# Performance work log

Hardware: AMD Instinct MI355X
Metric: run time of the kernel (lower is better)

The kernel has to match this reference:

```python
import jax, jax.numpy as jnp
import numpy as np

B, T, C, HS = 4, 2048, 2048, 64
H = C // HS
LW, LA, LV, LG = 64, 64, 32, 128
EPS_GN = 0.00064


def setup_inputs() -> dict:
    key = jax.random.key(0)
    ks = jax.random.split(key, 32)
    rn = lambda k, shape, s=1.0: jax.random.normal(k, shape, dtype=jnp.float32) * s
    return {
        "x": rn(ks[0], (B, T, C)),
        "v_first": rn(ks[1], (B, T, C)),
        "x_prev": rn(ks[2], (B, C)),
        "wkv_state": rn(ks[3], (B, H, HS, HS), 0.1),
        "x_r": rn(ks[4], (C,), 0.1),
        "x_w": rn(ks[5], (C,), 0.1),
        "x_k": rn(ks[6], (C,), 0.1),
        "x_v": rn(ks[7], (C,), 0.1),
        "x_a": rn(ks[8], (C,), 0.1),
        "x_g": rn(ks[9], (C,), 0.1),
        "w0": rn(ks[10], (C,), 0.1),
        "w1": rn(ks[11], (C, LW), 0.02),
        "w2": rn(ks[12], (LW, C), 0.02),
        "a0": rn(ks[13], (C,), 0.1),
        "a1": rn(ks[14], (C, LA), 0.02),
        "a2": rn(ks[15], (LA, C), 0.02),
        "v0": rn(ks[16], (C,), 0.1),
        "v1": rn(ks[17], (C, LV), 0.02),
        "v2": rn(ks[18], (LV, C), 0.02),
        "g1": rn(ks[19], (C, LG), 0.02),
        "g2": rn(ks[20], (LG, C), 0.02),
        "k_k": rn(ks[21], (C,), 0.1),
        "k_a": rn(ks[22], (C,), 0.1),
        "r_k": rn(ks[23], (H, HS), 0.1),
        "Wr": rn(ks[24], (C, C), 0.02),
        "Wk": rn(ks[25], (C, C), 0.02),
        "Wv": rn(ks[26], (C, C), 0.02),
        "Wo": rn(ks[27], (C, C), 0.02),
        "ln_w": jnp.ones((C,), dtype=jnp.float32),
        "ln_b": jnp.zeros((C,), dtype=jnp.float32),
    }


def _fwd(x, v_first, x_prev, wkv_state, x_r, x_w, x_k, x_v, x_a, x_g,
         w0, w1, w2, a0, a1, a2, v0, v1, v2, g1, g2, k_k, k_a, r_k,
         Wr, Wk, Wv, Wo, ln_w, ln_b):
    Bb, Tt, Cc = x.shape
    # token shift
    xx = jnp.concatenate([x_prev[:, None, :], x[:, :-1, :]], axis=1) - x
    xr = x + xx * x_r; xw = x + xx * x_w; xk = x + xx * x_k
    xv = x + xx * x_v; xa = x + xx * x_a; xg = x + xx * x_g
    r = xr @ Wr
    k = xk @ Wk
    v = xv @ Wv
    # log-decay: -softplus(-(w0 + tanh(xw@w1)@w2)) - 0.5  (<= -0.5)
    w_raw = -jax.nn.softplus(-(w0 + jnp.tanh(xw @ w1) @ w2)) - 0.5
    # layer_id != 0: mix with v_first
    v = v + (v_first - v) * jax.nn.sigmoid(v0 + (xv @ v1) @ v2)
    a = jax.nn.sigmoid(a0 + (xa @ a1) @ a2)
    g = jax.nn.sigmoid(xg @ g1) @ g2
    kk = (k * k_k).reshape(Bb, Tt, H, HS)
    kk = kk / jnp.maximum(jnp.linalg.norm(kk, axis=-1, keepdims=True), 1e-12)
    k = k * (1.0 + (a - 1.0) * k_a)
    rh = r.reshape(Bb, Tt, H, HS)
    kh = k.reshape(Bb, Tt, H, HS)
    vh = v.reshape(Bb, Tt, H, HS)
    ah = -kk                                  # removal direction
    bh = kk * a.reshape(Bb, Tt, H, HS)        # insertion direction
    wd = jnp.exp(-jnp.exp(w_raw)).reshape(Bb, Tt, H, HS)  # decay in (0,1)
    def step(st, ts):
        r_t, w_t, k_t, v_t, a_t, b_t = ts     # each [B,H,N]
        sa = jnp.einsum('bhij,bhj->bhi', st, a_t)
        st = st * w_t[:, :, None, :] + sa[..., None] * b_t[:, :, None, :] \
             + v_t[..., None] * k_t[:, :, None, :]
        return st, jnp.einsum('bhij,bhj->bhi', st, r_t)
    xs = tuple(jnp.moveaxis(t, 1, 0) for t in (rh, wd, kh, vh, ah, bh))
    _, out = jax.lax.scan(step, wkv_state, xs)
    out = jnp.moveaxis(out, 0, 1)             # [B,T,H,N]
    # GroupNorm(H groups) over each head's N channels
    mu = out.mean(-1, keepdims=True)
    var = out.var(-1, keepdims=True)
    out = ((out - mu) * jax.lax.rsqrt(var + EPS_GN)).reshape(Bb, Tt, Cc) * ln_w + ln_b
    bonus = (rh * kh * r_k).sum(-1, keepdims=True) * vh
    out = out + bonus.reshape(Bb, Tt, Cc)
    return (out * g) @ Wo


def reference(x, v_first, x_prev, wkv_state, x_r, x_w, x_k, x_v, x_a, x_g,
              w0, w1, w2, a0, a1, a2, v0, v1, v2, g1, g2, k_k, k_a, r_k,
              Wr, Wk, Wv, Wo, ln_w, ln_b):
    return _fwd(x, v_first, x_prev, wkv_state, x_r, x_w, x_k, x_v, x_a, x_g,
                w0, w1, w2, a0, a1, a2, v0, v1, v2, g1, g2, k_k, k_a, r_k,
                Wr, Wk, Wv, Wo, ln_w, ln_b)
```

## Files before the change

kernel.cpp:

```cpp
#include <hip/hip_runtime.h>

typedef float f32x4 __attribute__((ext_vector_type(4)));
typedef __bf16 bf16x8 __attribute__((ext_vector_type(8)));
typedef unsigned int u32x4 __attribute__((ext_vector_type(4)));

#define DI __device__ __forceinline__

constexpr int B_ = 4, T_ = 2048, C_ = 2048, H_ = 32;
constexpr int M_ = B_ * T_;

DI unsigned short f2bf(float f) {
  unsigned u = __float_as_uint(f);
  return (unsigned short)((u + 0x7FFFu + ((u >> 16) & 1u)) >> 16);
}
DI float bf2f(unsigned short h) { return __uint_as_float(((unsigned)h) << 16); }

DI void gl16(const void* g, void* l) {
  __builtin_amdgcn_global_load_lds(
      (__attribute__((address_space(1))) const unsigned int*)g,
      (__attribute__((address_space(3))) unsigned int*)l, 16, 0, 0);
}

DI float qsum(float x) {
  int t = __builtin_amdgcn_update_dpp(0, __float_as_int(x), 0xB1, 0xF, 0xF, true);
  x += __int_as_float(t);
  t = __builtin_amdgcn_update_dpp(0, __float_as_int(x), 0x4E, 0xF, 0xF, true);
  return x + __int_as_float(t);
}

__global__ __launch_bounds__(256) void k_transpose(const float* __restrict__ in,
                                                   unsigned short* __restrict__ out,
                                                   int R, int C) {
  __shared__ float tile[32][33];
  int c0 = blockIdx.x * 32, r0 = blockIdx.y * 32;
  int tx = threadIdx.x & 31, ty = threadIdx.x >> 5;
#pragma unroll
  for (int i = 0; i < 4; ++i) {
    int r = r0 + ty * 4 + i, c = c0 + tx;
    if (r < R && c < C) tile[ty * 4 + i][tx] = in[(size_t)r * C + c];
  }
  __syncthreads();
#pragma unroll
  for (int i = 0; i < 4; ++i) {
    int c = c0 + ty * 4 + i, r = r0 + tx;
    if (r < R && c < C) out[(size_t)c * R + r] = f2bf(tile[tx][ty * 4 + i]);
  }
}

DI void mix_emit(const float* coef, int c0, size_t off,
                 const float* xv, const float* dx, unsigned short* dst) {
  unsigned short u[8];
#pragma unroll
  for (int i = 0; i < 2; ++i) {
    f32x4 cf = *(const f32x4*)(coef + c0 + i * 4);
#pragma unroll
    for (int j = 0; j < 4; ++j) u[i * 4 + j] = f2bf(xv[i * 4 + j] + dx[i * 4 + j] * cf[j]);
  }
  u32x4 pv;
#pragma unroll
  for (int j = 0; j < 4; ++j) pv[j] = (unsigned)u[2 * j] | ((unsigned)u[2 * j + 1] << 16);
  *(u32x4*)(dst + off) = pv;
}

__global__ __launch_bounds__(256) void k_prep3(
    const float* __restrict__ x, const float* __restrict__ xprev,
    const float* __restrict__ cR, const float* __restrict__ cV,
    const float* __restrict__ cK,
    unsigned short* __restrict__ XR, unsigned short* __restrict__ XV,
    unsigned short* __restrict__ XK) {
  int bt = blockIdx.x;
  int t = bt & (T_ - 1);
  int c0 = threadIdx.x * 8;
  size_t off = (size_t)bt * C_ + c0;
  const float* xp = x + off;
  const float* pp = t ? (xp - C_) : (xprev + (size_t)(bt >> 11) * C_ + c0);
  float xv[8], dx[8];
#pragma unroll
  for (int i = 0; i < 2; ++i) {
    f32x4 a = *(const f32x4*)(xp + i * 4);
    f32x4 p = *(const f32x4*)(pp + i * 4);
#pragma unroll
    for (int j = 0; j < 4; ++j) { xv[i * 4 + j] = a[j]; dx[i * 4 + j] = p[j] - a[j]; }
  }
  mix_emit(cR, c0, off, xv, dx, XR);
  mix_emit(cV, c0, off, xv, dx, XV);
  mix_emit(cK, c0, off, xv, dx, XK);
}

DI void stage_mix(const float* __restrict__ x, const float* __restrict__ xprev,
                  const float* __restrict__ coef, unsigned short* As,
                  int m0, int kt, int wv, int lane) {
  const int lr = lane >> 3, lc = (lane & 7) * 8;
  f32x4 c0 = *(const f32x4*)(coef + kt + lc);
  f32x4 c1 = *(const f32x4*)(coef + kt + lc + 4);
#pragma unroll
  for (int i = 0; i < 4; ++i) {
    int chunk = wv * 4 + i;
    int r = chunk * 8 + lr;
    int m = m0 + r;
    const float* xp = x + (size_t)m * C_ + kt + lc;
    const float* pp = (m & (T_ - 1)) ? (xp - C_)
                                     : (xprev + (size_t)(m >> 11) * C_ + kt + lc);
    f32x4 xv0 = *(const f32x4*)xp, xv1 = *(const f32x4*)(xp + 4);
    f32x4 pv0 = *(const f32x4*)pp, pv1 = *(const f32x4*)(pp + 4);
    unsigned short u[8];
#pragma unroll
    for (int j = 0; j < 4; ++j) u[j] = f2bf(xv0[j] + (pv0[j] - xv0[j]) * c0[j]);
#pragma unroll
    for (int j = 0; j < 4; ++j) u[4 + j] = f2bf(xv1[j] + (pv1[j] - xv1[j]) * c1[j]);
    u32x4 pk;
#pragma unroll
    for (int j = 0; j < 4; ++j) pk[j] = (unsigned)u[2 * j] | ((unsigned)u[2 * j + 1] << 16);
    *(u32x4*)((char*)As + chunk * 1024 + lane * 16) = pk;
  }
}

template <int EPI>
__global__ __launch_bounds__(256, 2) void k_gemm_big(
    const unsigned short* __restrict__ A,
    const unsigned short* __restrict__ Bt,
    float* __restrict__ outF, unsigned short* __restrict__ outB,
    const unsigned short* __restrict__ svb, const float* __restrict__ vfirst,
    const unsigned short* __restrict__ abf,
    const float* __restrict__ k_k, const float* __restrict__ k_a,
    unsigned short* __restrict__ ahb, unsigned short* __restrict__ bhb) {
  __shared__ __align__(16) unsigned short As[128][64];
  __shared__ __align__(16) unsigned short Bs[128][64];
  const int tid = threadIdx.x, lane = tid & 63, wv = tid >> 6;
  const int bid = blockIdx.x;
  const int loc = bid >> 3;
  const int by = (bid & 7) * 8 + (loc & 7);
  const int bx = loc >> 3;
  const int m0 = by * 128, n0 = bx * 128;
  const int wm = (wv >> 1) * 64, wn = (wv & 1) * 64;
  const int lr = lane >> 3, lc = (lane & 7) * 8;
  f32x4 acc[4][4] = {};
  for (int kt = 0; kt < C_; kt += 64) {
    __syncthreads();
#pragma unroll
    for (int i = 0; i < 4; ++i) {
      int chunk = wv * 4 + i, r = chunk * 8 + lr;
      gl16(A + (size_t)(m0 + r) * C_ + kt + lc, (char*)&As[0][0] + chunk * 1024);
      gl16(Bt + (size_t)(n0 + r) * C_ + kt + lc, (char*)&Bs[0][0] + chunk * 1024);
    }
    __syncthreads();
    const int rr = lane & 15;
#pragma unroll
    for (int kh = 0; kh < 2; ++kh) {
      const int kof = kh * 32 + (lane >> 4) * 8;
      bf16x8 af[4], bfv[4];
#pragma unroll
      for (int i = 0; i < 4; ++i) af[i] = *(const bf16x8*)&As[wm + i * 16 + rr][kof];
#pragma unroll
      for (int j = 0; j < 4; ++j) bfv[j] = *(const bf16x8*)&Bs[wn + j * 16 + rr][kof];
#pragma unroll
      for (int i = 0; i < 4; ++i)
#pragma unroll
        for (int j = 0; j < 4; ++j)
          acc[i][j] = __builtin_amdgcn_mfma_f32_16x16x32_bf16(af[i], bfv[j], acc[i][j], 0, 0, 0);
    }
  }
  const int cr = (lane >> 4) * 4, cc2 = lane & 15;
  if constexpr (EPI == 2) {
    float kkv[4], kav[4];
#pragma unroll
    for (int j = 0; j < 4; ++j) {
      int col = n0 + wn + j * 16 + cc2;
      kkv[j] = k_k[col];
      kav[j] = k_a[col];
    }
#pragma unroll
    for (int i = 0; i < 4; ++i)
#pragma unroll
      for (int q = 0; q < 4; ++q) {
        int row = m0 + wm + i * 16 + cr + q;
        float kk4[4], p = 0.f;
#pragma unroll
        for (int j = 0; j < 4; ++j) {
          float kkc = acc[i][j][q] * kkv[j];
          kk4[j] = kkc;
          p += kkc * kkc;
        }
        p += __shfl_xor(p, 1); p += __shfl_xor(p, 2);
        p += __shfl_xor(p, 4); p += __shfl_xor(p, 8);
        float inv = 1.f / fmaxf(sqrtf(p), 1e-12f);
#pragma unroll
        for (int j = 0; j < 4; ++j) {
          int col = n0 + wn + j * 16 + cc2;
          size_t off = (size_t)row * C_ + col;
          float kkn = kk4[j] * inv;
          float a = bf2f(abf[off]);
          ahb[off] = f2bf(-kkn);
          bhb[off] = f2bf(kkn * a);
          outB[off] = f2bf(acc[i][j][q] * (1.f + (a - 1.f) * kav[j]));
        }
      }
  } else {
#pragma unroll
    for (int i = 0; i < 4; ++i)
#pragma unroll
      for (int j = 0; j < 4; ++j)
#pragma unroll
        for (int q = 0; q < 4; ++q) {
          int row = m0 + wm + i * 16 + cr + q;
          int col = n0 + wn + j * 16 + cc2;
          size_t off = (size_t)row * C_ + col;
          float v = acc[i][j][q];
          if constexpr (EPI == 0) {
            outB[off] = f2bf(v);
          } else if constexpr (EPI == 1) {
            float s = bf2f(svb[off]);
            outB[off] = f2bf(v + (vfirst[off] - v) * s);
          } else {
            outF[off] = v;
          }
        }
  }
}

template <int N, int ACT, bool FUSED>
DI void down_body(int m0, unsigned short (*As)[64], unsigned short (*Bs)[64],
                  const unsigned short* __restrict__ A,
                  const float* __restrict__ x, const float* __restrict__ xprev,
                  const float* __restrict__ coef, const unsigned short* __restrict__ Bt,
                  unsigned short* __restrict__ out) {
  const int tid = threadIdx.x, lane = tid & 63, wv = tid >> 6;
  const int wm = wv * 32;
  const int lr = lane >> 3, lc = (lane & 7) * 8;
  f32x4 acc[2][N / 16] = {};
  for (int kt = 0; kt < C_; kt += 64) {
    __syncthreads();
    if constexpr (FUSED) {
      stage_mix(x, xprev, coef, &As[0][0], m0, kt, wv, lane);
    } else {
#pragma unroll
      for (int i = 0; i < 4; ++i) {
        int chunk = wv * 4 + i, r = chunk * 8 + lr;
        gl16(A + (size_t)(m0 + r) * C_ + kt + lc, (char*)&As[0][0] + chunk * 1024);
      }
    }
#pragma unroll
    for (int i = 0; i < N / 32; ++i) {
      int chunk = wv * (N / 32) + i, r = chunk * 8 + lr;
      gl16(Bt + (size_t)r * C_ + kt + lc, (char*)&Bs[0][0] + chunk * 1024);
    }
    __syncthreads();
    const int rr = lane & 15;
#pragma unroll
    for (int kh = 0; kh < 2; ++kh) {
      const int kof = kh * 32 + (lane >> 4) * 8;
      bf16x8 af[2], bfv[N / 16];
#pragma unroll
      for (int i = 0; i < 2; ++i) af[i] = *(const bf16x8*)&As[wm + i * 16 + rr][kof];
#pragma unroll
      for (int j = 0; j < N / 16; ++j) bfv[j] = *(const bf16x8*)&Bs[j * 16 + rr][kof];
#pragma unroll
      for (int i = 0; i < 2; ++i)
#pragma unroll
        for (int j = 0; j < N / 16; ++j)
          acc[i][j] = __builtin_amdgcn_mfma_f32_16x16x32_bf16(af[i], bfv[j], acc[i][j], 0, 0, 0);
    }
  }
  const int cr = (lane >> 4) * 4, cc2 = lane & 15;
#pragma unroll
  for (int i = 0; i < 2; ++i)
#pragma unroll
    for (int j = 0; j < N / 16; ++j)
#pragma unroll
      for (int q = 0; q < 4; ++q) {
        int row = m0 + wm + i * 16 + cr + q;
        int col = j * 16 + cc2;
        float v = acc[i][j][q];
        if (ACT == 1) v = tanhf(v);
        else if (ACT == 2) v = 1.f / (1.f + expf(-v));
        out[(size_t)row * N + col] = f2bf(v);
      }
}

__global__ __launch_bounds__(256, 2) void k_down4(
    const float* __restrict__ x, const float* __restrict__ xprev,
    const unsigned short* __restrict__ XMv,
    const float* __restrict__ xw, const float* __restrict__ xa,
    const float* __restrict__ xg,
    const unsigned short* __restrict__ W1T, const unsigned short* __restrict__ A1T,
    const unsigned short* __restrict__ V1T, const unsigned short* __restrict__ G1T,
    unsigned short* __restrict__ HWB, unsigned short* __restrict__ HAB,
    unsigned short* __restrict__ HVB, unsigned short* __restrict__ HGB) {
  __shared__ __align__(16) unsigned short As[128][64];
  __shared__ __align__(16) unsigned short Bs[128][64];
  int g = blockIdx.x >> 6;
  int m0 = (blockIdx.x & 63) * 128;
  if (g == 0)      down_body<64, 1, true>(m0, As, Bs, nullptr, x, xprev, xw, W1T, HWB);
  else if (g == 1) down_body<64, 0, true>(m0, As, Bs, nullptr, x, xprev, xa, A1T, HAB);
  else if (g == 2) down_body<32, 0, false>(m0, As, Bs, XMv, nullptr, nullptr, nullptr, V1T, HVB);
  else             down_body<128, 2, true>(m0, As, Bs, nullptr, x, xprev, xg, G1T, HGB);
}

template <int K, int MODE>
__global__ __launch_bounds__(256, 2) void k_up(
    const unsigned short* __restrict__ A, const unsigned short* __restrict__ Bt,
    const float* __restrict__ bias, float* __restrict__ outF,
    unsigned short* __restrict__ outB) {
  __shared__ __align__(16) unsigned short As[128][K];
  __shared__ __align__(16) unsigned short Bs[128][K];
  const int tid = threadIdx.x, lane = tid & 63, wv = tid >> 6;
  const int m0 = blockIdx.y * 128, n0 = blockIdx.x * 128;
  const int wm = (wv >> 1) * 64, wn = (wv & 1) * 64;
  constexpr int LPR = K / 8;
  constexpr int RPC = 64 / LPR;
  const int lr = lane / LPR, lc = (lane % LPR) * 8;
  f32x4 acc[4][4] = {};
#pragma unroll
  for (int i = 0; i < K / 16; ++i) {
    int chunk = wv * (K / 16) + i;
    int r = chunk * RPC + lr;
    gl16(A + (size_t)(m0 + r) * K + lc, (char*)&As[0][0] + chunk * 1024);
    gl16(Bt + (size_t)(n0 + r) * K + lc, (char*)&Bs[0][0] + chunk * 1024);
  }
  __syncthreads();
  const int rr = lane & 15;
#pragma unroll
  for (int ks = 0; ks < K / 32; ++ks) {
    const int kof = ks * 32 + (lane >> 4) * 8;
    bf16x8 af[4], bfv[4];
#pragma unroll
    for (int i = 0; i < 4; ++i) af[i] = *(const bf16x8*)&As[wm + i * 16 + rr][kof];
#pragma unroll
    for (int j = 0; j < 4; ++j) bfv[j] = *(const bf16x8*)&Bs[wn + j * 16 + rr][kof];
#pragma unroll
    for (int i = 0; i < 4; ++i)
#pragma unroll
      for (int j = 0; j < 4; ++j)
        acc[i][j] = __builtin_amdgcn_mfma_f32_16x16x32_bf16(af[i], bfv[j], acc[i][j], 0, 0, 0);
  }
  const int cr = (lane >> 4) * 4, cc2 = lane & 15;
#pragma unroll
  for (int i = 0; i < 4; ++i)
#pragma unroll
    for (int j = 0; j < 4; ++j)
#pragma unroll
      for (int q = 0; q < 4; ++q) {
        int row = m0 + wm + i * 16 + cr + q;
        int col = n0 + wn + j * 16 + cc2;
        size_t off = (size_t)row * C_ + col;
        float up = acc[i][j][q];
        if (MODE == 0) {
          float z = -(bias[col] + up);
          float sp = fmaxf(z, 0.f) + log1pf(expf(-fabsf(z)));
          outF[off] = expf(-expf(-sp - 0.5f));
        } else if (MODE == 1) {
          outB[off] = f2bf(1.f / (1.f + expf(-(bias[col] + up))));
        } else {
          outB[off] = f2bf(up);
        }
      }
}

__global__ __launch_bounds__(64) void k_scan(
    const unsigned short* __restrict__ RB, const float* __restrict__ WD,
    const unsigned short* __restrict__ KB, const unsigned short* __restrict__ VB,
    const unsigned short* __restrict__ AHB, const unsigned short* __restrict__ BHB,
    const float* __restrict__ s0, float* __restrict__ out) {
  const int lane = threadIdx.x & 63;
  const int p = blockIdx.x;
  const int wr = p >> 7, bh = p & 127;
  const int b = bh >> 5, h = bh & 31;
  const int e = lane & 7, rl = lane >> 3;
  const int row = wr * 8 + rl;
  const int e8 = e * 8;
  const size_t base = (size_t)b * T_ * C_ + h * 64;
  float S[8];
  {
    const float* sp = s0 + ((size_t)(b * H_ + h) * 64 + row) * 64 + e8;
    f32x4 s0v = *(const f32x4*)sp, s1v = *(const f32x4*)(sp + 4);
#pragma unroll
    for (int j = 0; j < 4; ++j) { S[j] = s0v[j]; S[4 + j] = s1v[j]; }
  }

#define DECL_SLOT(n) bf16x8 r##n, k##n, a##n, bb##n; f32x4 wA##n, wB##n; unsigned short v##n;
  DECL_SLOT(0) DECL_SLOT(1) DECL_SLOT(2) DECL_SLOT(3)

#define ISSUE(n, t)                                              \
  {                                                              \
    int ti = (t) < T_ ? (t) : T_ - 1;                            \
    size_t eo = base + (size_t)ti * C_;                          \
    size_t ee = eo + e8;                                         \
    r##n = *(const bf16x8*)(RB + ee);                            \
    k##n = *(const bf16x8*)(KB + ee);                            \
    a##n = *(const bf16x8*)(AHB + ee);                           \
    bb##n = *(const bf16x8*)(BHB + ee);                          \
    wA##n = *(const f32x4*)(WD + ee);                            \
    wB##n = *(const f32x4*)(WD + ee + 4);                        \
    v##n = VB[eo + row];                                         \
  }

#define STEP(n, t)                                               \
  {                                                              \
    float rr[8], kk[8], aa[8], bv[8], ww[8];                     \
    _Pragma("unroll") for (int j = 0; j < 8; ++j) {              \
      rr[j] = (float)r##n[j];                                    \
      kk[j] = (float)k##n[j];                                    \
      aa[j] = (float)a##n[j];                                    \
      bv[j] = (float)bb##n[j];                                   \
    }                                                            \
    _Pragma("unroll") for (int j = 0; j < 4; ++j) {              \
      ww[j] = wA##n[j];                                          \
      ww[4 + j] = wB##n[j];                                      \
    }                                                            \
    float sa0 = S[0] * aa[0], sa1 = S[1] * aa[1];                \
    _Pragma("unroll") for (int j = 2; j < 8; j += 2) {           \
      sa0 = fmaf(S[j], aa[j], sa0);                              \
      sa1 = fmaf(S[j + 1], aa[j + 1], sa1);                      \
    }                                                            \
    float sa = qsum(sa0 + sa1);                                  \
    sa += __shfl_xor(sa, 4);                                     \
    float vi = bf2f(v##n);                                       \
    float o0 = 0.f, o1 = 0.f;                                    \
    _Pragma("unroll") for (int j = 0; j < 8; j += 2) {           \
      S[j] = fmaf(S[j], ww[j], fmaf(sa, bv[j], vi * kk[j]));     \
      S[j + 1] = fmaf(S[j + 1], ww[j + 1],                       \
                      fmaf(sa, bv[j + 1], vi * kk[j + 1]));      \
      o0 = fmaf(S[j], rr[j], o0);                                \
      o1 = fmaf(S[j + 1], rr[j + 1], o1);                        \
    }                                                            \
    float o = qsum(o0 + o1);                                     \
    o += __shfl_xor(o, 4);                                       \
    if (e == 0) out[base + (size_t)(t) * C_ + row] = o;          \
  }

  ISSUE(0, 0) ISSUE(1, 1) ISSUE(2, 2)
#pragma unroll 1
  for (int t = 0; t < T_; t += 4) {
    ISSUE(3, t + 3) STEP(0, t)
    ISSUE(0, t + 4) STEP(1, t + 1)
    ISSUE(1, t + 5) STEP(2, t + 2)
    ISSUE(2, t + 6) STEP(3, t + 3)
  }
#undef DECL_SLOT
#undef ISSUE
#undef STEP
}

__global__ __launch_bounds__(256) void k_gn(
    const float* __restrict__ o, const unsigned short* __restrict__ rb,
    const unsigned short* __restrict__ kb, const unsigned short* __restrict__ v,
    const unsigned short* __restrict__ g, const float* __restrict__ r_k,
    const float* __restrict__ lnw, const float* __restrict__ lnb,
    unsigned short* __restrict__ outg) {
  int wid = blockIdx.x * 4 + (threadIdx.x >> 6);
  int lane = threadIdx.x & 63;
  int h = wid & (H_ - 1);
  size_t bt = (size_t)(wid >> 5);
  size_t off = bt * C_ + h * 64 + lane;
  int c = h * 64 + lane;
  float x = o[off];
  float mu = x;
#pragma unroll
  for (int m = 1; m < 64; m <<= 1) mu += __shfl_xor(mu, m);
  mu *= (1.f / 64.f);
  float d = x - mu;
  float var = d * d;
#pragma unroll
  for (int m = 1; m < 64; m <<= 1) var += __shfl_xor(var, m);
  var *= (1.f / 64.f);
  float y = d * rsqrtf(var + 6.4e-4f) * lnw[c] + lnb[c];
  float bd = bf2f(rb[off]) * bf2f(kb[off]) * r_k[c];
#pragma unroll
  for (int m = 1; m < 64; m <<= 1) bd += __shfl_xor(bd, m);
  float res = (y + bd * bf2f(v[off])) * bf2f(g[off]);
  outg[off] = f2bf(res);
}

extern "C" void kernel_launch(void* const* d_in, const int* in_sizes, int n_in,
                              void* d_out, int out_size, void* d_ws, size_t ws_size,
                              hipStream_t stream) {
  const float* x      = (const float*)d_in[0];
  const float* vfirst = (const float*)d_in[1];
  const float* xprev  = (const float*)d_in[2];
  const float* wkv0   = (const float*)d_in[3];
  const float* x_r = (const float*)d_in[4];
  const float* x_w = (const float*)d_in[5];
  const float* x_k = (const float*)d_in[6];
  const float* x_v = (const float*)d_in[7];
  const float* x_a = (const float*)d_in[8];
  const float* x_g = (const float*)d_in[9];
  const float* w0 = (const float*)d_in[10];
  const float* w1 = (const float*)d_in[11];
  const float* w2 = (const float*)d_in[12];
  const float* a0 = (const float*)d_in[13];
  const float* a1 = (const float*)d_in[14];
  const float* a2 = (const float*)d_in[15];
  const float* v0 = (const float*)d_in[16];
  const float* v1 = (const float*)d_in[17];
  const float* v2 = (const float*)d_in[18];
  const float* g1 = (const float*)d_in[19];
  const float* g2 = (const float*)d_in[20];
  const float* k_k = (const float*)d_in[21];
  const float* k_a = (const float*)d_in[22];
  const float* r_k = (const float*)d_in[23];
  const float* Wr = (const float*)d_in[24];
  const float* Wk = (const float*)d_in[25];
  const float* Wv = (const float*)d_in[26];
  const float* Wo = (const float*)d_in[27];
  const float* lnw = (const float*)d_in[28];
  const float* lnb = (const float*)d_in[29];
  float* out = (float*)d_out;
  char* ws = (char*)d_ws;

  size_t woff = 0;
  auto alloc = [&](size_t n) { char* p = ws + woff; woff += n; return p; };
  char* R1 = alloc(67108864);
  unsigned short* ABF = (unsigned short*)R1;
  unsigned short* SVB = (unsigned short*)(R1 + 33554432);
  float* WD = (float*)R1;
  unsigned short* WT  = (unsigned short*)alloc(8388608);
  unsigned short* W1T = (unsigned short*)alloc(262144);
  unsigned short* A1T = (unsigned short*)alloc(262144);
  unsigned short* V1T = (unsigned short*)alloc(131072);
  unsigned short* G1T = (unsigned short*)alloc(524288);
  unsigned short* W2T = (unsigned short*)alloc(262144);
  unsigned short* A2T = (unsigned short*)alloc(262144);
  unsigned short* V2T = (unsigned short*)alloc(131072);
  unsigned short* G2T = (unsigned short*)alloc(524288);
  unsigned short* HWB = (unsigned short*)alloc(1048576);
  unsigned short* HAB = (unsigned short*)alloc(1048576);
  unsigned short* HVB = (unsigned short*)alloc(524288);
  unsigned short* HGB = (unsigned short*)alloc(2097152);
  unsigned short* RB  = (unsigned short*)alloc(33554432);
  unsigned short* KB  = (unsigned short*)alloc(33554432);
  unsigned short* VB  = (unsigned short*)alloc(33554432);
  unsigned short* AHB = (unsigned short*)alloc(33554432);
  unsigned short* BHB = (unsigned short*)alloc(33554432);
  alloc(65536);
  unsigned short* XMr = VB;
  unsigned short* XMv = KB;
  unsigned short* XMk = (unsigned short*)out;
  unsigned short* GBF  = AHB;
  unsigned short* OUTG = BHB;

  dim3 blk(256);
  dim3 gg(16, 64);
  dim3 g1d(1024);

  k_transpose<<<dim3(2, 64), blk, 0, stream>>>(w1, W1T, 2048, 64);
  k_transpose<<<dim3(2, 64), blk, 0, stream>>>(a1, A1T, 2048, 64);
  k_transpose<<<dim3(1, 64), blk, 0, stream>>>(v1, V1T, 2048, 32);
  k_transpose<<<dim3(4, 64), blk, 0, stream>>>(g1, G1T, 2048, 128);
  k_transpose<<<dim3(64, 2), blk, 0, stream>>>(w2, W2T, 64, 2048);
  k_transpose<<<dim3(64, 2), blk, 0, stream>>>(a2, A2T, 64, 2048);
  k_transpose<<<dim3(64, 1), blk, 0, stream>>>(v2, V2T, 32, 2048);
  k_transpose<<<dim3(64, 4), blk, 0, stream>>>(g2, G2T, 128, 2048);

  k_prep3<<<dim3(M_), blk, 0, stream>>>(x, xprev, x_r, x_v, x_k, XMr, XMv, XMk);

  k_down4<<<dim3(256), blk, 0, stream>>>(x, xprev, XMv, x_w, x_a, x_g,
                                         W1T, A1T, V1T, G1T, HWB, HAB, HVB, HGB);

  k_up<64, 1><<<gg, blk, 0, stream>>>(HAB, A2T, a0, nullptr, ABF);
  k_up<32, 1><<<gg, blk, 0, stream>>>(HVB, V2T, v0, nullptr, SVB);

  k_transpose<<<dim3(64, 64), blk, 0, stream>>>(Wr, WT, 2048, 2048);
  k_gemm_big<0><<<g1d, blk, 0, stream>>>(XMr, WT,
      nullptr, RB, nullptr, nullptr, nullptr, nullptr, nullptr, nullptr, nullptr);

  k_transpose<<<dim3(64, 64), blk, 0, stream>>>(Wv, WT, 2048, 2048);
  k_gemm_big<1><<<g1d, blk, 0, stream>>>(XMv, WT,
      nullptr, VB, SVB, vfirst, nullptr, nullptr, nullptr, nullptr, nullptr);

  k_transpose<<<dim3(64, 64), blk, 0, stream>>>(Wk, WT, 2048, 2048);
  k_gemm_big<2><<<g1d, blk, 0, stream>>>(XMk, WT,
      nullptr, KB, nullptr, nullptr, ABF, k_k, k_a, AHB, BHB);

  k_up<64, 0><<<gg, blk, 0, stream>>>(HWB, W2T, w0, WD, nullptr);

  k_scan<<<dim3(1024), dim3(64), 0, stream>>>(RB, WD, KB, VB, AHB, BHB, wkv0, out);

  k_up<128, 3><<<gg, blk, 0, stream>>>(HGB, G2T, nullptr, nullptr, GBF);

  k_gn<<<dim3(65536), blk, 0, stream>>>(out, RB, KB, VB, GBF, r_k, lnw, lnb, OUTG);

  k_transpose<<<dim3(64, 64), blk, 0, stream>>>(Wo, WT, 2048, 2048);
  k_gemm_big<3><<<g1d, blk, 0, stream>>>(OUTG, WT,
      out, nullptr, nullptr, nullptr, nullptr, nullptr, nullptr, nullptr, nullptr);
}
```

Before: 1.411 ms.

## Precompute all six token-shift mixes in prep kernel, merge small transposes, use DPP row reduction

Moves the w/a/g token-shift mixing out of the low-rank down-projection kernel into the prep kernel, which now writes six bf16 mixed inputs. k_down4 then loads those with direct global-to-LDS copies instead of recomputing from fp32 x and x_prev on every k-tile. The eight small weight transposes become one launch, and the scan's 8-lane reduction replaces a cross-lane shuffle with a third DPP step (row_shr-style control). This costs extra bf16 writes and reads for three more activation buffers, which reuse scratch space, in exchange for a simpler down-projection inner loop and fewer launches.

```diff
diff --git a/kernel.cpp b/kernel.cpp
--- a/kernel.cpp
+++ b/kernel.cpp
@@ -21,30 +21,55 @@
       (__attribute__((address_space(3))) unsigned int*)l, 16, 0, 0);
 }
 
-DI float qsum(float x) {
+DI float rsum8(float x) {
   int t = __builtin_amdgcn_update_dpp(0, __float_as_int(x), 0xB1, 0xF, 0xF, true);
   x += __int_as_float(t);
   t = __builtin_amdgcn_update_dpp(0, __float_as_int(x), 0x4E, 0xF, 0xF, true);
-  return x + __int_as_float(t);
+  x += __int_as_float(t);
+  t = __builtin_amdgcn_update_dpp(0, __float_as_int(x), 0x141, 0xF, 0xF, true);
+  x += __int_as_float(t);
+  return x;
+}
+
+DI void tr_body(const float* __restrict__ in, unsigned short* __restrict__ out,
+                int R, int C, int bx, int by, float (*tile)[33]) {
+  int c0 = bx * 32, r0 = by * 32;
+  int tx = threadIdx.x & 31, ty = threadIdx.x >> 5;
+#pragma unroll
+  for (int i = 0; i < 4; ++i) {
+    int r = r0 + ty * 4 + i, c = c0 + tx;
+    if (r < R && c < C) tile[ty * 4 + i][tx] = in[(size_t)r * C + c];
+  }
+  __syncthreads();
+#pragma unroll
+  for (int i = 0; i < 4; ++i) {
+    int c = c0 + ty * 4 + i, r = r0 + tx;
+    if (r < R && c < C) out[(size_t)c * R + r] = f2bf(tile[tx][ty * 4 + i]);
+  }
 }
 
 __global__ __launch_bounds__(256) void k_transpose(const float* __restrict__ in,
                                                    unsigned short* __restrict__ out,
                                                    int R, int C) {
   __shared__ float tile[32][33];
-  int c0 = blockIdx.x * 32, r0 = blockIdx.y * 32;
-  int tx = threadIdx.x & 31, ty = threadIdx.x >> 5;
-#pragma unroll
-  for (int i = 0; i < 4; ++i) {
-    int r = r0 + ty * 4 + i, c = c0 + tx;
-    if (r < R && c < C) tile[ty * 4 + i][tx] = in[(size_t)r * C + c];
-  }
-  __syncthreads();
-#pragma unroll
-  for (int i = 0; i < 4; ++i) {
-    int c = c0 + ty * 4 + i, r = r0 + tx;
-    if (r < R && c < C) out[(size_t)c * R + r] = f2bf(tile[tx][ty * 4 + i]);
-  }
+  tr_body(in, out, R, C, blockIdx.x, blockIdx.y, tile);
+}
+
+__global__ __launch_bounds__(256) void k_transpose8(
+    const float* w1, unsigned short* W1T, const float* a1, unsigned short* A1T,
+    const float* v1, unsigned short* V1T, const float* g1, unsigned short* G1T,
+    const float* w2, unsigned short* W2T, const float* a2, unsigned short* A2T,
+    const float* v2, unsigned short* V2T, const float* g2, unsigned short* G2T) {
+  __shared__ float tile[32][33];
+  int b = blockIdx.x;
+  if (b < 128)       tr_body(w1, W1T, 2048, 64, b % 2, b / 2, tile);
+  else if (b < 256)  { b -= 128; tr_body(a1, A1T, 2048, 64, b % 2, b / 2, tile); }
+  else if (b < 320)  { b -= 256; tr_body(v1, V1T, 2048, 32, 0, b, tile); }
+  else if (b < 576)  { b -= 320; tr_body(g1, G1T, 2048, 128, b % 4, b / 4, tile); }
+  else if (b < 704)  { b -= 576; tr_body(w2, W2T, 64, 2048, b % 64, b / 64, tile); }
+  else if (b < 832)  { b -= 704; tr_body(a2, A2T, 64, 2048, b % 64, b / 64, tile); }
+  else if (b < 896)  { b -= 832; tr_body(v2, V2T, 32, 2048, b % 64, b / 64, tile); }
+  else               { b -= 896; tr_body(g2, G2T, 128, 2048, b % 64, b / 64, tile); }
 }
 
 DI void mix_emit(const float* coef, int c0, size_t off,
@@ -62,12 +87,14 @@
   *(u32x4*)(dst + off) = pv;
 }
 
-__global__ __launch_bounds__(256) void k_prep3(
+__global__ __launch_bounds__(256) void k_prep6(
     const float* __restrict__ x, const float* __restrict__ xprev,
     const float* __restrict__ cR, const float* __restrict__ cV,
-    const float* __restrict__ cK,
+    const float* __restrict__ cK, const float* __restrict__ cW,
+    const float* __restrict__ cA, const float* __restrict__ cG,
     unsigned short* __restrict__ XR, unsigned short* __restrict__ XV,
-    unsigned short* __restrict__ XK) {
+    unsigned short* __restrict__ XK, unsigned short* __restrict__ XW,
+    unsigned short* __restrict__ XA, unsigned short* __restrict__ XG) {
   int bt = blockIdx.x;
   int t = bt & (T_ - 1);
   int c0 = threadIdx.x * 8;
@@ -85,34 +112,9 @@
   mix_emit(cR, c0, off, xv, dx, XR);
   mix_emit(cV, c0, off, xv, dx, XV);
   mix_emit(cK, c0, off, xv, dx, XK);
-}
-
-DI void stage_mix(const float* __restrict__ x, const float* __restrict__ xprev,
-                  const float* __restrict__ coef, unsigned short* As,
-                  int m0, int kt, int wv, int lane) {
-  const int lr = lane >> 3, lc = (lane & 7) * 8;
-  f32x4 c0 = *(const f32x4*)(coef + kt + lc);
-  f32x4 c1 = *(const f32x4*)(coef + kt + lc + 4);
-#pragma unroll
-  for (int i = 0; i < 4; ++i) {
-    int chunk = wv * 4 + i;
-    int r = chunk * 8 + lr;
-    int m = m0 + r;
-    const float* xp = x + (size_t)m * C_ + kt + lc;
-    const float* pp = (m & (T_ - 1)) ? (xp - C_)
-                                     : (xprev + (size_t)(m >> 11) * C_ + kt + lc);
-    f32x4 xv0 = *(const f32x4*)xp, xv1 = *(const f32x4*)(xp + 4);
-    f32x4 pv0 = *(const f32x4*)pp, pv1 = *(const f32x4*)(pp + 4);
-    unsigned short u[8];
-#pragma unroll
-    for (int j = 0; j < 4; ++j) u[j] = f2bf(xv0[j] + (pv0[j] - xv0[j]) * c0[j]);
-#pragma unroll
-    for (int j = 0; j < 4; ++j) u[4 + j] = f2bf(xv1[j] + (pv1[j] - xv1[j]) * c1[j]);
-    u32x4 pk;
-#pragma unroll
-    for (int j = 0; j < 4; ++j) pk[j] = (unsigned)u[2 * j] | ((unsigned)u[2 * j + 1] << 16);
-    *(u32x4*)((char*)As + chunk * 1024 + lane * 16) = pk;
-  }
+  mix_emit(cW, c0, off, xv, dx, XW);
+  mix_emit(cA, c0, off, xv, dx, XA);
+  mix_emit(cG, c0, off, xv, dx, XG);
 }
 
 template <int EPI>
@@ -218,11 +220,10 @@
   }
 }
 
-template <int N, int ACT, bool FUSED>
+template <int N, int ACT>
 DI void down_body(int m0, unsigned short (*As)[64], unsigned short (*Bs)[64],
                   const unsigned short* __restrict__ A,
-                  const float* __restrict__ x, const float* __restrict__ xprev,
-                  const float* __restrict__ coef, const unsigned short* __restrict__ Bt,
+                  const unsigned short* __restrict__ Bt,
                   unsigned short* __restrict__ out) {
   const int tid = threadIdx.x, lane = tid & 63, wv = tid >> 6;
   const int wm = wv * 32;
@@ -230,14 +231,10 @@
   f32x4 acc[2][N / 16] = {};
   for (int kt = 0; kt < C_; kt += 64) {
     __syncthreads();
-    if constexpr (FUSED) {
-      stage_mix(x, xprev, coef, &As[0][0], m0, kt, wv, lane);
-    } else {
-#pragma unroll
-      for (int i = 0; i < 4; ++i) {
-        int chunk = wv * 4 + i, r = chunk * 8 + lr;
-        gl16(A + (size_t)(m0 + r) * C_ + kt + lc, (char*)&As[0][0] + chunk * 1024);
-      }
+#pragma unroll
+    for (int i = 0; i < 4; ++i) {
+      int chunk = wv * 4 + i, r = chunk * 8 + lr;
+      gl16(A + (size_t)(m0 + r) * C_ + kt + lc, (char*)&As[0][0] + chunk * 1024);
     }
 #pragma unroll
     for (int i = 0; i < N / 32; ++i) {
@@ -278,10 +275,8 @@
 }
 
 __global__ __launch_bounds__(256, 2) void k_down4(
-    const float* __restrict__ x, const float* __restrict__ xprev,
-    const unsigned short* __restrict__ XMv,
-    const float* __restrict__ xw, const float* __restrict__ xa,
-    const float* __restrict__ xg,
+    const unsigned short* __restrict__ XMw, const unsigned short* __restrict__ XMa,
+    const unsigned short* __restrict__ XMv, const unsigned short* __restrict__ XMg,
     const unsigned short* __restrict__ W1T, const unsigned short* __restrict__ A1T,
     const unsigned short* __restrict__ V1T, const unsigned short* __restrict__ G1T,
     unsigned short* __restrict__ HWB, unsigned short* __restrict__ HAB,
@@ -290,10 +285,10 @@
   __shared__ __align__(16) unsigned short Bs[128][64];
   int g = blockIdx.x >> 6;
   int m0 = (blockIdx.x & 63) * 128;
-  if (g == 0)      down_body<64, 1, true>(m0, As, Bs, nullptr, x, xprev, xw, W1T, HWB);
-  else if (g == 1) down_body<64, 0, true>(m0, As, Bs, nullptr, x, xprev, xa, A1T, HAB);
-  else if (g == 2) down_body<32, 0, false>(m0, As, Bs, XMv, nullptr, nullptr, nullptr, V1T, HVB);
-  else             down_body<128, 2, true>(m0, As, Bs, nullptr, x, xprev, xg, G1T, HGB);
+  if (g == 0)      down_body<64, 1>(m0, As, Bs, XMw, W1T, HWB);
+  else if (g == 1) down_body<64, 0>(m0, As, Bs, XMa, A1T, HAB);
+  else if (g == 2) down_body<32, 0>(m0, As, Bs, XMv, V1T, HVB);
+  else             down_body<128, 2>(m0, As, Bs, XMg, G1T, HGB);
 }
 
 template <int K, int MODE>
@@ -356,7 +351,7 @@
       }
 }
 
-__global__ __launch_bounds__(64) void k_scan(
+__global__ __launch_bounds__(64, 1) void k_scan(
     const unsigned short* __restrict__ RB, const float* __restrict__ WD,
     const unsigned short* __restrict__ KB, const unsigned short* __restrict__ VB,
     const unsigned short* __restrict__ AHB, const unsigned short* __restrict__ BHB,
@@ -412,8 +407,7 @@
       sa0 = fmaf(S[j], aa[j], sa0);                              \
       sa1 = fmaf(S[j + 1], aa[j + 1], sa1);                      \
     }                                                            \
-    float sa = qsum(sa0 + sa1);                                  \
-    sa += __shfl_xor(sa, 4);                                     \
+    float sa = rsum8(sa0 + sa1);                                 \
     float vi = bf2f(v##n);                                       \
     float o0 = 0.f, o1 = 0.f;                                    \
     _Pragma("unroll") for (int j = 0; j < 8; j += 2) {           \
@@ -423,8 +417,7 @@
       o0 = fmaf(S[j], rr[j], o0);                                \
       o1 = fmaf(S[j + 1], rr[j + 1], o1);                        \
     }                                                            \
-    float o = qsum(o0 + o1);                                     \
-    o += __shfl_xor(o, 4);                                       \
+    float o = rsum8(o0 + o1);                                    \
     if (e == 0) out[base + (size_t)(t) * C_ + row] = o;          \
   }
 
@@ -535,6 +528,9 @@
   unsigned short* XMr = VB;
   unsigned short* XMv = KB;
   unsigned short* XMk = (unsigned short*)out;
+  unsigned short* XMw = AHB;
+  unsigned short* XMa = BHB;
+  unsigned short* XMg = RB;
   unsigned short* GBF  = AHB;
   unsigned short* OUTG = BHB;
 
@@ -542,18 +538,13 @@
   dim3 gg(16, 64);
   dim3 g1d(1024);
 
-  k_transpose<<<dim3(2, 64), blk, 0, stream>>>(w1, W1T, 2048, 64);
-  k_transpose<<<dim3(2, 64), blk, 0, stream>>>(a1, A1T, 2048, 64);
-  k_transpose<<<dim3(1, 64), blk, 0, stream>>>(v1, V1T, 2048, 32);
-  k_transpose<<<dim3(4, 64), blk, 0, stream>>>(g1, G1T, 2048, 128);
-  k_transpose<<<dim3(64, 2), blk, 0, stream>>>(w2, W2T, 64, 2048);
-  k_transpose<<<dim3(64, 2), blk, 0, stream>>>(a2, A2T, 64, 2048);
-  k_transpose<<<dim3(64, 1), blk, 0, stream>>>(v2, V2T, 32, 2048);
-  k_transpose<<<dim3(64, 4), blk, 0, stream>>>(g2, G2T, 128, 2048);
-
-  k_prep3<<<dim3(M_), blk, 0, stream>>>(x, xprev, x_r, x_v, x_k, XMr, XMv, XMk);
-
-  k_down4<<<dim3(256), blk, 0, stream>>>(x, xprev, XMv, x_w, x_a, x_g,
+  k_transpose8<<<dim3(1152), blk, 0, stream>>>(w1, W1T, a1, A1T, v1, V1T, g1, G1T,
+                                               w2, W2T, a2, A2T, v2, V2T, g2, G2T);
+
+  k_prep6<<<dim3(M_), blk, 0, stream>>>(x, xprev, x_r, x_v, x_k, x_w, x_a, x_g,
+                                        XMr, XMv, XMk, XMw, XMa, XMg);
+
+  k_down4<<<dim3(256), blk, 0, stream>>>(XMw, XMa, XMv, XMg,
                                          W1T, A1T, V1T, G1T, HWB, HAB, HVB, HGB);
 
   k_up<64, 1><<<gg, blk, 0, stream>>>(HAB, A2T, a0, nullptr, ABF);
```

Result: faster. 1.361 ms (-3.5%).
